# Kernel tuning notes

Hardware: AMD Instinct MI355X
Metric: run time of the kernel (lower is better)

## Reference

```python
import jax, jax.numpy as jnp
import numpy as np

RANK = 16
ALPHA = 16.0
IN_F = 4096
OUT_F = 11008
TOKENS = 64


def setup_inputs() -> dict:
    key = jax.random.key(0)
    k_x, k_w, k_s, k_a, k_b, k_bias = jax.random.split(key, 6)
    return {
        "x": jax.random.normal(k_x, (TOKENS, IN_F), dtype=jnp.float32),
        "weight_int4": jax.random.normal(k_w, (OUT_F, IN_F), dtype=jnp.float32),
        "weight_scale": jax.random.uniform(k_s, (OUT_F,), dtype=jnp.float32),
        "lora_A": jax.random.normal(k_a, (RANK, IN_F), dtype=jnp.float32) * 0.01,
        "lora_B": jax.random.normal(k_b, (OUT_F, RANK), dtype=jnp.float32),
        "bias": jax.random.normal(k_bias, (OUT_F,), dtype=jnp.float32),
    }


def reference(x, weight_int4, weight_scale, lora_A, lora_B, bias):
    # Dequantize: per-output-channel scale.  [out, in]
    weight = weight_int4 * weight_scale[:, None]
    # LoRA delta: B @ A scaled by alpha/rank.  [out, in]
    lora_weight = (lora_B @ lora_A) * (ALPHA / RANK)
    effective_weight = weight + lora_weight
    # F.linear: x @ W^T + b  ->  [tokens, out]
    return x @ effective_weight.T + bias
```

## Files before the change

### kernel.cpp

```cpp
#include <hip/hip_runtime.h>
#include <hip/hip_bf16.h>
#include <cstdint>

#define TOK   64
#define INF   4096
#define OUTF  11008
#define KCHUNKS 128
#define QCNT  16
#define KC    8
#define NBLK2 86

using bf16x8  = __attribute__((ext_vector_type(8))) __bf16;
using floatx4 = __attribute__((ext_vector_type(4))) float;

union B8u { uint32_t u[4]; uint4 q; bf16x8 v; };

__device__ __forceinline__ uint32_t hi2(float a, float b) {
    return (__float_as_uint(a) >> 16) | (__float_as_uint(b) & 0xffff0000u);
}
__device__ __forceinline__ float losub(float x) {
    return x - __uint_as_float(__float_as_uint(x) & 0xffff0000u);
}
__device__ __forceinline__ void packW(float4 a, float4 b, B8u& wh, B8u& wl) {
    wh.u[0] = hi2(a.x, a.y);  wh.u[1] = hi2(a.z, a.w);
    wh.u[2] = hi2(b.x, b.y);  wh.u[3] = hi2(b.z, b.w);
    wl.u[0] = hi2(losub(a.x), losub(a.y));
    wl.u[1] = hi2(losub(a.z), losub(a.w));
    wl.u[2] = hi2(losub(b.x), losub(b.y));
    wl.u[3] = hi2(losub(b.z), losub(b.w));
}

__global__ __launch_bounds__(256) void k_prep_x(const float* __restrict__ x,
        unsigned short* __restrict__ xh, unsigned short* __restrict__ xl) {
    int idx  = blockIdx.x * 256 + threadIdx.x;
    int j    = idx & 7;
    int lane = (idx >> 3) & 63;
    int kc   = (idx >> 9) & 127;
    int mt   = idx >> 16;
    int row  = mt * 16 + (lane & 15);
    int col  = kc * 32 + ((lane >> 4) << 3) + j;
    float v  = x[(size_t)row * INF + col];
    uint32_t u = __float_as_uint(v);
    float lo = losub(v);
    xh[idx] = (unsigned short)(u >> 16);
    xl[idx] = (unsigned short)(__float_as_uint(lo) >> 16);
}

__global__ __launch_bounds__(256) void k_lora_t(const float* __restrict__ x,
        const float* __restrict__ A, float* __restrict__ tm) {
    int t = blockIdx.x, wv = threadIdx.x >> 6, lane = threadIdx.x & 63;
    int r = blockIdx.y * 4 + wv;
    const float4* xr = (const float4*)(x + (size_t)t * INF);
    const float4* ar = (const float4*)(A + (size_t)r * INF);
    float s = 0.f;
#pragma unroll
    for (int i = 0; i < INF / 4 / 64; ++i) {
        float4 a = xr[lane + i * 64], b = ar[lane + i * 64];
        s += a.x * b.x + a.y * b.y + a.z * b.z + a.w * b.w;
    }
#pragma unroll
    for (int off = 32; off > 0; off >>= 1) s += __shfl_down(s, off);
    if (lane == 0) tm[t * 16 + r] = s;
}

template<bool ATOMIC>
__global__ __launch_bounds__(256, 2) void k_main(const float* __restrict__ W,
        const uint4* __restrict__ xh, const uint4* __restrict__ xl,
        const float* __restrict__ scale, float* __restrict__ part,
        float* __restrict__ out) {
    __shared__ uint4 xs[2][4][KC][64];

    int tid  = threadIdx.x;
    int lane = tid & 63;
    int wv   = tid >> 6;
    int nb   = blockIdx.x % NBLK2;
    int q    = blockIdx.x / NBLK2;
    int quad = lane >> 4;
    int ch0  = nb * 128 + wv * 32 + (lane & 15);

#pragma unroll
    for (int i = 0; i < 16; ++i) {
        int c  = wv * 16 + i;
        int hl = c >> 5, mt = (c >> 3) & 3, kc = c & 7;
        const uint4* g = (hl ? xl : xh)
                       + ((size_t)mt * KCHUNKS + q * KC + kc) * 64 + lane;
        __builtin_amdgcn_global_load_lds(
            (const __attribute__((address_space(1))) uint32_t*)g,
            (__attribute__((address_space(3))) uint32_t*)&xs[hl][mt][kc][0],
            16, 0, 0);
    }
    __syncthreads();

    const float* wp0 = W + (size_t)ch0 * INF + q * (KC * 32) + quad * 8;
    const float* wp1 = wp0 + (size_t)16 * INF;
    float4 w0a[KC], w0b[KC], w1a[KC], w1b[KC];
#pragma unroll
    for (int kc = 0; kc < KC; ++kc) {
        w0a[kc] = *(const float4*)(wp0 + kc * 32);
        w0b[kc] = *(const float4*)(wp0 + kc * 32 + 4);
        w1a[kc] = *(const float4*)(wp1 + kc * 32);
        w1b[kc] = *(const float4*)(wp1 + kc * 32 + 4);
    }

    floatx4 acc0[4] = {}, acc1[4] = {};

#pragma unroll
    for (int kc = 0; kc < KC; ++kc) {
        B8u wh0, wl0, wh1, wl1;
        packW(w0a[kc], w0b[kc], wh0, wl0);
        packW(w1a[kc], w1b[kc], wh1, wl1);
#pragma unroll
        for (int mt = 0; mt < 4; ++mt) {
            B8u ah, al;
            ah.q = xs[0][mt][kc][lane];
            al.q = xs[1][mt][kc][lane];
            acc0[mt] = __builtin_amdgcn_mfma_f32_16x16x32_bf16(ah.v, wh0.v, acc0[mt], 0, 0, 0);
            acc0[mt] = __builtin_amdgcn_mfma_f32_16x16x32_bf16(ah.v, wl0.v, acc0[mt], 0, 0, 0);
            acc0[mt] = __builtin_amdgcn_mfma_f32_16x16x32_bf16(al.v, wh0.v, acc0[mt], 0, 0, 0);
            acc1[mt] = __builtin_amdgcn_mfma_f32_16x16x32_bf16(ah.v, wh1.v, acc1[mt], 0, 0, 0);
            acc1[mt] = __builtin_amdgcn_mfma_f32_16x16x32_bf16(ah.v, wl1.v, acc1[mt], 0, 0, 0);
            acc1[mt] = __builtin_amdgcn_mfma_f32_16x16x32_bf16(al.v, wh1.v, acc1[mt], 0, 0, 0);
        }
    }

#pragma unroll
    for (int mt = 0; mt < 4; ++mt) {
        int token = mt * 16 + quad * 4;
#pragma unroll
        for (int r = 0; r < 4; ++r) {
            if constexpr (ATOMIC) {
                atomicAdd(&out[(size_t)(token + r) * OUTF + ch0], scale[ch0] * acc0[mt][r]);
                atomicAdd(&out[(size_t)(token + r) * OUTF + ch0 + 16], scale[ch0 + 16] * acc1[mt][r]);
            } else {
                part[((size_t)q * TOK + token + r) * OUTF + ch0]      = acc0[mt][r];
                part[((size_t)q * TOK + token + r) * OUTF + ch0 + 16] = acc1[mt][r];
            }
        }
    }
}

__global__ __launch_bounds__(256) void k_post(const float* __restrict__ part,
        const float* __restrict__ scale, const float* __restrict__ bias,
        const float* __restrict__ lB, const float* __restrict__ tm,
        float* __restrict__ out) {
    int o = blockIdx.x * 256 + threadIdx.x;
    int t = blockIdx.y;
    if (o >= OUTF) return;
    float s = 0.f;
#pragma unroll
    for (int qq = 0; qq < QCNT; ++qq)
        s += part[((size_t)qq * TOK + t) * OUTF + o];
    const float4* Br = (const float4*)(lB + (size_t)o * 16);
    const float4* tr = (const float4*)(tm + (size_t)t * 16);
    float l = 0.f;
#pragma unroll
    for (int i = 0; i < 4; ++i) {
        float4 b = Br[i], tt = tr[i];
        l += b.x * tt.x + b.y * tt.y + b.z * tt.z + b.w * tt.w;
    }
    out[(size_t)t * OUTF + o] = s * scale[o] + l + bias[o];
}

__global__ __launch_bounds__(256) void k_pre(const float* __restrict__ bias,
        const float* __restrict__ lB, const float* __restrict__ tm,
        float* __restrict__ out) {
    int o = blockIdx.x * 256 + threadIdx.x;
    int t = blockIdx.y;
    if (o >= OUTF) return;
    const float4* Br = (const float4*)(lB + (size_t)o * 16);
    const float4* tr = (const float4*)(tm + (size_t)t * 16);
    float l = 0.f;
#pragma unroll
    for (int i = 0; i < 4; ++i) {
        float4 b = Br[i], tt = tr[i];
        l += b.x * tt.x + b.y * tt.y + b.z * tt.z + b.w * tt.w;
    }
    out[(size_t)t * OUTF + o] = l + bias[o];
}

extern "C" void kernel_launch(void* const* d_in, const int* in_sizes, int n_in,
                              void* d_out, int out_size, void* d_ws, size_t ws_size,
                              hipStream_t stream) {
    const float* x     = (const float*)d_in[0];
    const float* W     = (const float*)d_in[1];
    const float* scale = (const float*)d_in[2];
    const float* lA    = (const float*)d_in[3];
    const float* lB    = (const float*)d_in[4];
    const float* bias  = (const float*)d_in[5];
    float* out = (float*)d_out;

    char* ws = (char*)d_ws;
    unsigned short* xh = (unsigned short*)(ws);
    unsigned short* xl = (unsigned short*)(ws + 524288);
    float* tm   = (float*)(ws + 1048576);
    float* part = (float*)(ws + 1052672);
    const size_t need = 1052672 + (size_t)QCNT * TOK * OUTF * 4;

    k_prep_x<<<1024, 256, 0, stream>>>(x, xh, xl);
    k_lora_t<<<dim3(TOK, 4), 256, 0, stream>>>(x, lA, tm);

    if (ws_size >= need) {
        k_main<false><<<NBLK2 * QCNT, 256, 0, stream>>>(W, (const uint4*)xh,
                (const uint4*)xl, scale, part, out);
        k_post<<<dim3(43, TOK), 256, 0, stream>>>(part, scale, bias, lB, tm, out);
    } else {
        k_pre<<<dim3(43, TOK), 256, 0, stream>>>(bias, lB, tm, out);
        k_main<true><<<NBLK2 * QCNT, 256, 0, stream>>>(W, (const uint4*)xh,
                (const uint4*)xl, scale, nullptr, out);
    }
}
```

Measured before the change: 298.8 us.

## Stage weights through LDS with swizzled async loads and a 4-phase K loop

The main GEMM kernel now stages both the fp32 weight tile and the split-bf16 activations in LDS, using global_load_lds with a rotated (swizzled) layout so each wave reads contiguous weight rows coalesced. Before, each thread loaded weights straight into registers. Each block now covers 64 channels and 512 K elements in four phases, with the K split going from 16 to 8. The aim is better coalescing of the dominant weight stream, fewer registers and a smaller partial-sum buffer for the reduction. In exchange it adds per-phase barriers and has no double buffering, so load latency is exposed on every phase.

New measurement: 272.8 us. -8.7%, faster.

```diff
diff --git a/kernel.cpp b/kernel.cpp
--- a/kernel.cpp
+++ b/kernel.cpp
@@ -6,9 +6,8 @@
 #define INF   4096
 #define OUTF  11008
 #define KCHUNKS 128
-#define QCNT  16
-#define KC    8
-#define NBLK2 86
+#define QCNT  8
+#define NCHB  172
 
 using bf16x8  = __attribute__((ext_vector_type(8))) __bf16;
 using floatx4 = __attribute__((ext_vector_type(4))) float;
@@ -68,58 +67,68 @@
         const uint4* __restrict__ xh, const uint4* __restrict__ xl,
         const float* __restrict__ scale, float* __restrict__ part,
         float* __restrict__ out) {
-    __shared__ uint4 xs[2][4][KC][64];
+    __shared__ uint4 wlds[2048];
+    __shared__ uint4 xsl[2048];
 
     int tid  = threadIdx.x;
     int lane = tid & 63;
     int wv   = tid >> 6;
-    int nb   = blockIdx.x % NBLK2;
-    int q    = blockIdx.x / NBLK2;
     int quad = lane >> 4;
-    int ch0  = nb * 128 + wv * 32 + (lane & 15);
-
-#pragma unroll
-    for (int i = 0; i < 16; ++i) {
-        int c  = wv * 16 + i;
-        int hl = c >> 5, mt = (c >> 3) & 3, kc = c & 7;
-        const uint4* g = (hl ? xl : xh)
-                       + ((size_t)mt * KCHUNKS + q * KC + kc) * 64 + lane;
-        __builtin_amdgcn_global_load_lds(
-            (const __attribute__((address_space(1))) uint32_t*)g,
-            (__attribute__((address_space(3))) uint32_t*)&xs[hl][mt][kc][0],
-            16, 0, 0);
-    }
-    __syncthreads();
-
-    const float* wp0 = W + (size_t)ch0 * INF + q * (KC * 32) + quad * 8;
-    const float* wp1 = wp0 + (size_t)16 * INF;
-    float4 w0a[KC], w0b[KC], w1a[KC], w1b[KC];
-#pragma unroll
-    for (int kc = 0; kc < KC; ++kc) {
-        w0a[kc] = *(const float4*)(wp0 + kc * 32);
-        w0b[kc] = *(const float4*)(wp0 + kc * 32 + 4);
-        w1a[kc] = *(const float4*)(wp1 + kc * 32);
-        w1b[kc] = *(const float4*)(wp1 + kc * 32 + 4);
-    }
-
-    floatx4 acc0[4] = {}, acc1[4] = {};
-
-#pragma unroll
-    for (int kc = 0; kc < KC; ++kc) {
-        B8u wh0, wl0, wh1, wl1;
-        packW(w0a[kc], w0b[kc], wh0, wl0);
-        packW(w1a[kc], w1b[kc], wh1, wl1);
-#pragma unroll
-        for (int mt = 0; mt < 4; ++mt) {
-            B8u ah, al;
-            ah.q = xs[0][mt][kc][lane];
-            al.q = xs[1][mt][kc][lane];
-            acc0[mt] = __builtin_amdgcn_mfma_f32_16x16x32_bf16(ah.v, wh0.v, acc0[mt], 0, 0, 0);
-            acc0[mt] = __builtin_amdgcn_mfma_f32_16x16x32_bf16(ah.v, wl0.v, acc0[mt], 0, 0, 0);
-            acc0[mt] = __builtin_amdgcn_mfma_f32_16x16x32_bf16(al.v, wh0.v, acc0[mt], 0, 0, 0);
-            acc1[mt] = __builtin_amdgcn_mfma_f32_16x16x32_bf16(ah.v, wh1.v, acc1[mt], 0, 0, 0);
-            acc1[mt] = __builtin_amdgcn_mfma_f32_16x16x32_bf16(ah.v, wl1.v, acc1[mt], 0, 0, 0);
-            acc1[mt] = __builtin_amdgcn_mfma_f32_16x16x32_bf16(al.v, wh1.v, acc1[mt], 0, 0, 0);
+    int nb   = blockIdx.x % NCHB;
+    int q    = blockIdx.x / NCHB;
+    int chl  = wv * 16 + (lane & 15);
+    int ch   = nb * 64 + chl;
+
+    const int kbase = q * 512;
+    int rpar = lane >> 5;
+    int gg   = lane & 31;
+
+    floatx4 acc[4] = {};
+
+    for (int ph = 0; ph < 4; ++ph) {
+        __syncthreads();
+
+#pragma unroll
+        for (int t = 0; t < 8; ++t) {
+            int i = wv * 8 + t;
+            int r = i * 2 + rpar;
+            int f = (gg - r) & 31;
+            const float* src = W + (size_t)(nb * 64 + r) * INF
+                             + kbase + ph * 128 + f * 4;
+            __builtin_amdgcn_global_load_lds(
+                (const __attribute__((address_space(1))) uint32_t*)src,
+                (__attribute__((address_space(3))) uint32_t*)&wlds[i * 64],
+                16, 0, 0);
+        }
+#pragma unroll
+        for (int t = 0; t < 8; ++t) {
+            int j  = wv * 8 + t;
+            int hl = j >> 4, mt = (j >> 2) & 3, kc = j & 3;
+            const uint4* src = (hl ? xl : xh)
+                + ((size_t)(mt * KCHUNKS + q * 16 + ph * 4 + kc) * 64 + lane);
+            __builtin_amdgcn_global_load_lds(
+                (const __attribute__((address_space(1))) uint32_t*)src,
+                (__attribute__((address_space(3))) uint32_t*)&xsl[j * 64],
+                16, 0, 0);
+        }
+        __syncthreads();
+
+#pragma unroll
+        for (int kc = 0; kc < 4; ++kc) {
+            int f0 = (kc * 4 + quad) * 2;
+            uint4 wf0 = wlds[chl * 32 + ((f0 + chl) & 31)];
+            uint4 wf1 = wlds[chl * 32 + ((f0 + 1 + chl) & 31)];
+            B8u wh, wl;
+            packW(*(float4*)&wf0, *(float4*)&wf1, wh, wl);
+#pragma unroll
+            for (int mt = 0; mt < 4; ++mt) {
+                B8u ah, al;
+                ah.q = xsl[(mt * 4 + kc) * 64 + lane];
+                al.q = xsl[(16 + mt * 4 + kc) * 64 + lane];
+                acc[mt] = __builtin_amdgcn_mfma_f32_16x16x32_bf16(ah.v, wh.v, acc[mt], 0, 0, 0);
+                acc[mt] = __builtin_amdgcn_mfma_f32_16x16x32_bf16(ah.v, wl.v, acc[mt], 0, 0, 0);
+                acc[mt] = __builtin_amdgcn_mfma_f32_16x16x32_bf16(al.v, wh.v, acc[mt], 0, 0, 0);
+            }
         }
     }
 
@@ -129,11 +138,9 @@
 #pragma unroll
         for (int r = 0; r < 4; ++r) {
             if constexpr (ATOMIC) {
-                atomicAdd(&out[(size_t)(token + r) * OUTF + ch0], scale[ch0] * acc0[mt][r]);
-                atomicAdd(&out[(size_t)(token + r) * OUTF + ch0 + 16], scale[ch0 + 16] * acc1[mt][r]);
+                atomicAdd(&out[(size_t)(token + r) * OUTF + ch], scale[ch] * acc[mt][r]);
             } else {
-                part[((size_t)q * TOK + token + r) * OUTF + ch0]      = acc0[mt][r];
-                part[((size_t)q * TOK + token + r) * OUTF + ch0 + 16] = acc1[mt][r];
+                part[((size_t)q * TOK + token + r) * OUTF + ch] = acc[mt][r];
             }
         }
     }
@@ -200,12 +207,12 @@
     k_lora_t<<<dim3(TOK, 4), 256, 0, stream>>>(x, lA, tm);
 
     if (ws_size >= need) {
-        k_main<false><<<NBLK2 * QCNT, 256, 0, stream>>>(W, (const uint4*)xh,
+        k_main<false><<<NCHB * QCNT, 256, 0, stream>>>(W, (const uint4*)xh,
                 (const uint4*)xl, scale, part, out);
         k_post<<<dim3(43, TOK), 256, 0, stream>>>(part, scale, bias, lB, tm, out);
     } else {
         k_pre<<<dim3(43, TOK), 256, 0, stream>>>(bias, lB, tm, out);
-        k_main<true><<<NBLK2 * QCNT, 256, 0, stream>>>(W, (const uint4*)xh,
+        k_main<true><<<NCHB * QCNT, 256, 0, stream>>>(W, (const uint4*)xh,
                 (const uint4*)xl, scale, nullptr, out);
     }
 }
```
